# Kernel tuning notes

Hardware: AMD Instinct MI355X
Metric: run time of the kernel (lower is better)

Reference implementation:

```python
import jax, jax.numpy as jnp
import numpy as np

ALPHA = 1.0
ARAP_WEIGHT = 1.0
B, N, K, LATENT, HIDDEN = 16, 20000, 16, 256, 1024


def setup_inputs() -> dict:
    key = jax.random.key(0)
    ks = jax.random.split(key, 8)
    code = jax.random.normal(ks[0], (B, LATENT), jnp.float32)
    W1 = jax.random.normal(ks[1], (LATENT, HIDDEN), jnp.float32) / np.sqrt(LATENT)
    b1 = jnp.zeros((HIDDEN,), jnp.float32)
    W2 = jax.random.normal(ks[2], (HIDDEN, N * 3), jnp.float32) / np.sqrt(HIDDEN)
    b2 = jnp.zeros((N * 3,), jnp.float32)
    xyz1 = jax.random.normal(ks[3], (B, N, 3), jnp.float32)
    weightMatrix = jax.random.uniform(ks[4], (N, K), jnp.float32)
    area = jax.random.uniform(ks[5], (N,), jnp.float32)
    neighborsMatrix = jax.random.randint(ks[6], (N, K), 0, N, jnp.int32)
    numNeighbors = jax.random.randint(ks[7], (N,), 1, K + 1, jnp.int32)
    return {"code": code, "W1": W1, "b1": b1, "W2": W2, "b2": b2,
            "xyz1": xyz1, "weightMatrix": weightMatrix, "area": area,
            "neighborsMatrix": neighborsMatrix, "numNeighbors": numNeighbors}


def _mean_energy(code, W1, b1, W2, b2, xyz1, weightMatrix, area,
                 neighborsMatrix, numNeighbors):
    # decoder: MLP latent -> hidden -> N*3, reshaped to [B,N,3]
    h = jax.nn.relu(code @ W1 + b1)
    recon = (h @ W2 + b2).reshape(B, N, 3)

    # mask out padded neighbor slots, fold into weights  [N,K]
    mask = (jnp.arange(K)[None, :] < numNeighbors[:, None]).astype(jnp.float32)
    wm = weightMatrix * mask

    # neighbor-gathered edge vectors: rest pose d, deformed dq  [B,N,K,3]
    d = xyz1[:, :, None, :] - xyz1[:, neighborsMatrix, :]
    dq = recon[:, :, None, :] - recon[:, neighborsMatrix, :]

    # per-vertex weighted covariance and best-fit rotation (Procrustes)
    S = jnp.einsum('nk,bnki,bnkj->bnij', wm, d, dq)          # [B,N,3,3]
    U, s, Vt = jnp.linalg.svd(S)
    V = jnp.swapaxes(Vt, -1, -2)
    Ut = jnp.swapaxes(U, -1, -2)
    det = jnp.linalg.det(V @ Ut)                              # [B,N]
    Vf = V.at[..., :, -1].multiply(jnp.sign(det)[..., None])  # reflection fix
    R = jax.lax.stop_gradient(Vf @ Ut)                        # R treated as constant

    resid = dq - jnp.einsum('bnij,bnkj->bnki', R, d)          # [B,N,K,3]
    e = (ARAP_WEIGHT * ALPHA) * area[None, :, None] * wm[None] \
        * jnp.sum(resid * resid, axis=-1)                     # [B,N,K]
    # torch.mean(torch.mean(e, 2), 1)
    return jnp.mean(e, axis=(1, 2))                           # [B]


def reference(code, W1, b1, W2, b2, xyz1, weightMatrix, area,
              neighborsMatrix, numNeighbors):
    meanEnergy = _mean_energy(code, W1, b1, W2, b2, xyz1, weightMatrix, area,
                              neighborsMatrix, numNeighbors)
    # meanEnergy.backward(ones) -> grad of sum(meanEnergy) wrt code
    code_grad = jax.grad(lambda c: jnp.sum(
        _mean_energy(c, W1, b1, W2, b2, xyz1, weightMatrix, area,
                     neighborsMatrix, numNeighbors)))(code)
    return (meanEnergy, code_grad)
```

## Files before the change

### kernel.cpp

```cpp
#include <hip/hip_runtime.h>

constexpr int B_ = 16;
constexpr int NV = 20000;
constexpr int KN = 16;
constexpr int LAT = 256;
constexpr int HID = 1024;
constexpr int N3 = 60000;
constexpr int RCAP = 64;
constexpr int NCHUNK = 8;
constexpr float INV_NK = 1.0f / (20000.0f * 16.0f);

constexpr size_t H_OFF      = 0;
constexpr size_t XYZT_OFF   = H_OFF + B_ * HID;
constexpr size_t RECONT_OFF = XYZT_OFF + (size_t)N3 * 16;
constexpr size_t GRECON_OFF = RECONT_OFF + (size_t)N3 * 16;
constexpr size_t GH_OFF     = GRECON_OFF + (size_t)B_ * N3;
constexpr size_t RBUF_OFF   = GH_OFF + B_ * HID;
constexpr size_t RCOUNT_OFF = RBUF_OFF + (size_t)NV * 12 * 16;
constexpr size_t RLIST_OFF  = RCOUNT_OFF + NV;
constexpr size_t PART_OFF   = RLIST_OFF + (size_t)NV * RCAP;

__device__ __forceinline__ void atomAddF(float* p, float v) {
  unsafeAtomicAdd(p, v);
}

__global__ __launch_bounds__(256) void k_mlp1(
    const float* __restrict__ code, const float* __restrict__ W1,
    const float* __restrict__ b1, float* __restrict__ h) {
  int t = blockIdx.x * 256 + threadIdx.x;
  int b = t >> 10, hd = t & 1023;
  const float* c = code + b * LAT;
  float acc = b1[hd];
  #pragma unroll 4
  for (int l = 0; l < LAT; ++l) acc += c[l] * W1[l * HID + hd];
  h[t] = fmaxf(acc, 0.0f);
}

__global__ __launch_bounds__(256) void k_xpose(
    const float* __restrict__ xyz, float* __restrict__ xyzT) {
  __shared__ float sm[64][17];
  const int tid = threadIdx.x;
  const int n30 = blockIdx.x * 64;
  {
    const int n3l = tid & 63, bq = tid >> 6;
    #pragma unroll
    for (int p = 0; p < 4; ++p) {
      int b = p * 4 + bq;
      if (n30 + n3l < N3) sm[n3l][b] = xyz[(size_t)b * N3 + n30 + n3l];
    }
  }
  __syncthreads();
  {
    const int b = tid & 15, nq = tid >> 4;
    #pragma unroll
    for (int p = 0; p < 4; ++p) {
      int n3l = p * 16 + nq;
      if (n30 + n3l < N3) xyzT[(size_t)(n30 + n3l) * 16 + b] = sm[n3l][b];
    }
  }
}

__global__ __launch_bounds__(256) void k_mlp2(
    const float* __restrict__ h, const float* __restrict__ W2,
    float* __restrict__ part) {
  __shared__ float hs[16][128];
  const int tid = threadIdx.x;
  const int hd0 = blockIdx.y * 128;
  #pragma unroll
  for (int r = 0; r < 8; ++r) {
    int idx = r * 256 + tid;
    int bb = idx >> 7, cc = idx & 127;
    hs[bb][cc] = h[bb * HID + hd0 + cc];
  }
  __syncthreads();

  const int j4 = blockIdx.x * 1024 + tid * 4;
  if (j4 >= N3) return;

  float4 acc[16];
  #pragma unroll
  for (int b = 0; b < 16; ++b) acc[b] = make_float4(0.f, 0.f, 0.f, 0.f);

  const float* wp = W2 + (size_t)hd0 * N3 + j4;
  float4 w0 = *(const float4*)(wp);
  float4 w1 = *(const float4*)(wp + (size_t)N3);
  float4 w2 = *(const float4*)(wp + (size_t)2 * N3);
  float4 w3 = *(const float4*)(wp + (size_t)3 * N3);

  for (int g = 0; g < 32; ++g) {
    const float* np = wp + (size_t)4 * N3;
    float4 n0, n1, n2, n3;
    if (g < 31) {
      n0 = *(const float4*)(np);
      n1 = *(const float4*)(np + (size_t)N3);
      n2 = *(const float4*)(np + (size_t)2 * N3);
      n3 = *(const float4*)(np + (size_t)3 * N3);
    }
    #pragma unroll
    for (int b = 0; b < 16; ++b) {
      float4 hb = *(const float4*)&hs[b][g * 4];
      acc[b].x += hb.x * w0.x + hb.y * w1.x + hb.z * w2.x + hb.w * w3.x;
      acc[b].y += hb.x * w0.y + hb.y * w1.y + hb.z * w2.y + hb.w * w3.y;
      acc[b].z += hb.x * w0.z + hb.y * w1.z + hb.z * w2.z + hb.w * w3.z;
      acc[b].w += hb.x * w0.w + hb.y * w1.w + hb.z * w2.w + hb.w * w3.w;
    }
    wp = np; w0 = n0; w1 = n1; w2 = n2; w3 = n3;
  }

  float ac[4][16];
  #pragma unroll
  for (int b = 0; b < 16; ++b) {
    ac[0][b] = acc[b].x; ac[1][b] = acc[b].y;
    ac[2][b] = acc[b].z; ac[3][b] = acc[b].w;
  }
  float* pbase = part + ((size_t)blockIdx.y * N3 + j4) * 16;
  #pragma unroll
  for (int jj = 0; jj < 4; ++jj)
    #pragma unroll
    for (int q = 0; q < 4; ++q)
      *(float4*)(pbase + jj * 16 + q * 4) = make_float4(
          ac[jj][q*4+0], ac[jj][q*4+1], ac[jj][q*4+2], ac[jj][q*4+3]);
}

__global__ __launch_bounds__(256) void k_reduce(
    const float* __restrict__ part, const float* __restrict__ b2,
    float* __restrict__ reconT) {
  int t = blockIdx.x * 256 + threadIdx.x;
  if (t >= N3 * 16 / 4) return;
  size_t pos = (size_t)t * 4;
  int j = t >> 2;
  float4 s = *(const float4*)(part + pos);
  #pragma unroll
  for (int c = 1; c < NCHUNK; ++c) {
    float4 p = *(const float4*)(part + (size_t)c * N3 * 16 + pos);
    s.x += p.x; s.y += p.y; s.z += p.z; s.w += p.w;
  }
  float bias = b2[j];
  s.x += bias; s.y += bias; s.z += bias; s.w += bias;
  *(float4*)(reconT + pos) = s;
}

__global__ __launch_bounds__(256) void k_fill(
    const int* __restrict__ nbrs, const int* __restrict__ nnbr,
    int* __restrict__ rcount, int* __restrict__ rlist) {
  int e = blockIdx.x * 256 + threadIdx.x;
  int n = e >> 4, k = e & 15;
  if (k < nnbr[n]) {
    int v = nbrs[e];
    int slot = atomicAdd(&rcount[v], 1);
    if (slot < RCAP) rlist[v * RCAP + slot] = e;
  }
}

__global__ __launch_bounds__(256, 2) void k_rot(
    const float* __restrict__ xT, const float* __restrict__ qT,
    const float* __restrict__ wmat, const float* __restrict__ area,
    const int* __restrict__ nbrs, const int* __restrict__ nnbr,
    float* __restrict__ Rbuf, float* __restrict__ energy) {
  __shared__ float red[64];
  const int tid = threadIdx.x;
  const int b = tid & 15, nl = tid >> 4;
  const int n = blockIdx.x * 16 + nl;
  const int nn = nnbr[n];
  const float ar = area[n];
  const float x0 = xT[(size_t)n*48 + b],      x1 = xT[(size_t)n*48 + 16 + b],
              x2 = xT[(size_t)n*48 + 32 + b];
  const float q0 = qT[(size_t)n*48 + b],      q1 = qT[(size_t)n*48 + 16 + b],
              q2 = qT[(size_t)n*48 + 32 + b];

  float dX[KN], dY[KN], dZ[KN], eX[KN], eY[KN], eZ[KN], wk[KN];
  float S00=0,S01=0,S02=0,S10=0,S11=0,S12=0,S20=0,S21=0,S22=0;
  #pragma unroll
  for (int k = 0; k < KN; ++k) {
    float w=0, dx=0, dy=0, dz=0, ex=0, ey=0, ez=0;
    if (k < nn) {
      int m = nbrs[n * KN + k];
      w = wmat[n * KN + k];
      size_t mb = (size_t)m * 48 + b;
      dx = x0 - xT[mb]; dy = x1 - xT[mb + 16]; dz = x2 - xT[mb + 32];
      ex = q0 - qT[mb]; ey = q1 - qT[mb + 16]; ez = q2 - qT[mb + 32];
    }
    wk[k]=w; dX[k]=dx; dY[k]=dy; dZ[k]=dz; eX[k]=ex; eY[k]=ey; eZ[k]=ez;
    S00 += w*dx*ex; S01 += w*dx*ey; S02 += w*dx*ez;
    S10 += w*dy*ex; S11 += w*dy*ey; S12 += w*dy*ez;
    S20 += w*dz*ex; S21 += w*dz*ey; S22 += w*dz*ez;
  }

  float A00 = S00*S00 + S10*S10 + S20*S20;
  float A01 = S00*S01 + S10*S11 + S20*S21;
  float A02 = S00*S02 + S10*S12 + S20*S22;
  float A11 = S01*S01 + S11*S11 + S21*S21;
  float A12 = S01*S02 + S11*S12 + S21*S22;
  float A22 = S02*S02 + S12*S12 + S22*S22;
  float V00=1,V01=0,V02=0, V10=0,V11=1,V12=0, V20=0,V21=0,V22=1;

  auto rot = [&](float& app, float& aqq, float& apq, float& arp, float& arq,
                 float& vp0, float& vp1, float& vp2,
                 float& vq0, float& vq1, float& vq2) {
    float a = apq;
    if (fabsf(a) > 1e-37f) {
      float tau = (aqq - app) * 0.5f / a;
      float t = copysignf(1.0f, tau) / (fabsf(tau) + sqrtf(1.0f + tau * tau));
      float c = rsqrtf(1.0f + t * t);
      float s = t * c;
      float napp = c*c*app - 2.0f*s*c*a + s*s*aqq;
      float naqq = s*s*app + 2.0f*s*c*a + c*c*aqq;
      app = napp; aqq = naqq; apq = 0.0f;
      float rp = arp, rq = arq;
      arp = c*rp - s*rq; arq = s*rp + c*rq;
      float t0, t1;
      t0=vp0; t1=vq0; vp0 = c*t0 - s*t1; vq0 = s*t0 + c*t1;
      t0=vp1; t1=vq1; vp1 = c*t0 - s*t1; vq1 = s*t0 + c*t1;
      t0=vp2; t1=vq2; vp2 = c*t0 - s*t1; vq2 = s*t0 + c*t1;
    }
  };
  #pragma unroll
  for (int sweep = 0; sweep < 6; ++sweep) {
    rot(A00,A11,A01, A02,A12, V00,V10,V20, V01,V11,V21);
    rot(A00,A22,A02, A01,A12, V00,V10,V20, V02,V12,V22);
    rot(A11,A22,A12, A01,A02, V01,V11,V21, V02,V12,V22);
  }
  auto sw = [](float& a, float& c) { float t = a; a = c; c = t; };
  if (A00 < A11) { sw(A00,A11); sw(V00,V01); sw(V10,V11); sw(V20,V21); }
  if (A00 < A22) { sw(A00,A22); sw(V00,V02); sw(V10,V12); sw(V20,V22); }
  if (A11 < A22) { sw(A11,A22); sw(V01,V02); sw(V11,V12); sw(V21,V22); }

  float v1x=V00, v1y=V10, v1z=V20;
  float v2x=V01, v2y=V11, v2z=V21;

  float u1x = S00*v1x + S01*v1y + S02*v1z;
  float u1y = S10*v1x + S11*v1y + S12*v1z;
  float u1z = S20*v1x + S21*v1y + S22*v1z;
  float s1sq = u1x*u1x + u1y*u1y + u1z*u1z;
  if (s1sq > 1e-30f) { float r = rsqrtf(s1sq); u1x*=r; u1y*=r; u1z*=r; }
  else { u1x = 1.0f; u1y = 0.0f; u1z = 0.0f; }

  float u2x = S00*v2x + S01*v2y + S02*v2z;
  float u2y = S10*v2x + S11*v2y + S12*v2z;
  float u2z = S20*v2x + S21*v2y + S22*v2z;
  float pr = u2x*u1x + u2y*u1y + u2z*u1z;
  u2x -= pr*u1x; u2y -= pr*u1y; u2z -= pr*u1z;
  float s2sq = u2x*u2x + u2y*u2y + u2z*u2z;
  if (s2sq > 1e-12f * s1sq + 1e-30f) {
    float r = rsqrtf(s2sq); u2x*=r; u2y*=r; u2z*=r;
  } else {
    float ex_ = (fabsf(u1x) < 0.9f) ? 1.0f : 0.0f;
    float ey_ = 1.0f - ex_;
    float pp = ex_*u1x + ey_*u1y;
    u2x = ex_ - pp*u1x; u2y = ey_ - pp*u1y; u2z = -pp*u1z;
    float r = rsqrtf(u2x*u2x + u2y*u2y + u2z*u2z);
    u2x*=r; u2y*=r; u2z*=r;
  }
  float u3x = u1y*u2z - u1z*u2y, u3y = u1z*u2x - u1x*u2z, u3z = u1x*u2y - u1y*u2x;
  float v3x = v1y*v2z - v1z*v2y, v3y = v1z*v2x - v1x*v2z, v3z = v1x*v2y - v1y*v2x;

  float R00 = v1x*u1x + v2x*u2x + v3x*u3x;
  float R01 = v1x*u1y + v2x*u2y + v3x*u3y;
  float R02 = v1x*u1z + v2x*u2z + v3x*u3z;
  float R10 = v1y*u1x + v2y*u2x + v3y*u3x;
  float R11 = v1y*u1y + v2y*u2y + v3y*u3y;
  float R12 = v1y*u1z + v2y*u2z + v3y*u3z;
  float R20 = v1z*u1x + v2z*u2x + v3z*u3x;
  float R21 = v1z*u1y + v2z*u2y + v3z*u3y;
  float R22 = v1z*u1z + v2z*u2z + v3z*u3z;

  float esum = 0, go0 = 0, go1 = 0, go2 = 0;
  const float gf = 2.0f * ar * INV_NK;
  #pragma unroll
  for (int k = 0; k < KN; ++k) {
    float w = wk[k];
    float dx = dX[k], dy = dY[k], dz = dZ[k];
    float rx = eX[k] - (R00*dx + R01*dy + R02*dz);
    float ry = eY[k] - (R10*dx + R11*dy + R12*dz);
    float rz = eZ[k] - (R20*dx + R21*dy + R22*dz);
    esum += w * (rx*rx + ry*ry + rz*rz);
    float gc = gf * w;
    go0 += gc*rx; go1 += gc*ry; go2 += gc*rz;
  }
  esum *= ar * INV_NK;

  float* rb = Rbuf + (size_t)n * 192 + b;
  rb[0]=R00;  rb[16]=R01;  rb[32]=R02;
  rb[48]=R10; rb[64]=R11;  rb[80]=R12;
  rb[96]=R20; rb[112]=R21; rb[128]=R22;
  rb[144]=go0; rb[160]=go1; rb[176]=go2;

  esum += __shfl_down(esum, 32);
  esum += __shfl_down(esum, 16);
  int wave = tid >> 6, lane = tid & 63;
  if (lane < 16) red[wave * 16 + lane] = esum;
  __syncthreads();
  if (tid < 16) atomAddF(&energy[tid], red[tid] + red[16 + tid] + red[32 + tid] + red[48 + tid]);
}

__global__ __launch_bounds__(256) void k_scatter(
    const float* __restrict__ xT, const float* __restrict__ qT,
    const float* __restrict__ wmat, const float* __restrict__ area,
    const float* __restrict__ Rbuf, const int* __restrict__ rcount,
    const int* __restrict__ rlist, float* __restrict__ grecon) {
  int t = blockIdx.x * 256 + threadIdx.x;
  int v = t >> 4, b = t & 15;
  const float xv0 = xT[(size_t)v*48 + b], xv1 = xT[(size_t)v*48 + 16 + b],
              xv2 = xT[(size_t)v*48 + 32 + b];
  const float qv0 = qT[(size_t)v*48 + b], qv1 = qT[(size_t)v*48 + 16 + b],
              qv2 = qT[(size_t)v*48 + 32 + b];
  float g0 = 0, g1 = 0, g2 = 0;
  int deg = min(rcount[v], RCAP);
  for (int i = 0; i < deg; ++i) {
    int e = rlist[v * RCAP + i];
    int n = e >> 4;
    float gc = 2.0f * INV_NK * area[n] * wmat[e];
    const float* rb = Rbuf + (size_t)n * 192 + b;
    size_t nb = (size_t)n * 48 + b;
    float dx = xT[nb] - xv0, dy = xT[nb+16] - xv1, dz = xT[nb+32] - xv2;
    float ex = qT[nb] - qv0, ey = qT[nb+16] - qv1, ez = qT[nb+32] - qv2;
    float rx = ex - (rb[0]*dx  + rb[16]*dy  + rb[32]*dz);
    float ry = ey - (rb[48]*dx + rb[64]*dy  + rb[80]*dz);
    float rz = ez - (rb[96]*dx + rb[112]*dy + rb[128]*dz);
    g0 -= gc*rx; g1 -= gc*ry; g2 -= gc*rz;
  }
  const float* ob = Rbuf + (size_t)v * 192 + b;
  g0 += ob[144]; g1 += ob[160]; g2 += ob[176];
  float* gq = grecon + (size_t)b * N3 + v * 3;
  gq[0] = g0; gq[1] = g1; gq[2] = g2;
}

__global__ __launch_bounds__(256, 2) void k_mlp2_bwd(
    const float* __restrict__ gr, const float* __restrict__ W2,
    float* __restrict__ gh) {
  const int tid = threadIdx.x;
  const int lane = tid & 63;
  const int wv = tid >> 6;
  const int laneJ = lane & 15, laneR = lane >> 4;
  const int row0 = blockIdx.y * 32 + wv * 8 + laneR * 2;

  float4 acc0[16], acc1[16];
  #pragma unroll
  for (int b = 0; b < 16; ++b) {
    acc0[b] = make_float4(0.f, 0.f, 0.f, 0.f);
    acc1[b] = make_float4(0.f, 0.f, 0.f, 0.f);
  }

  const int jbase = blockIdx.x * 64 + laneJ * 4;
  const float* w2r0 = W2 + (size_t)row0 * N3;
  const float* w2r1 = W2 + (size_t)(row0 + 1) * N3;

  for (int it = 0; it < 59; ++it) {
    int j = jbase + it * 1024;
    if (j < N3) {
      float4 w0 = *(const float4*)(w2r0 + j);
      float4 w1 = *(const float4*)(w2r1 + j);
      #pragma unroll
      for (int b = 0; b < 16; ++b) {
        float4 g = *(const float4*)(gr + (size_t)b * N3 + j);
        acc0[b].x += g.x * w0.x; acc0[b].y += g.y * w0.y;
        acc0[b].z += g.z * w0.z; acc0[b].w += g.w * w0.w;
        acc1[b].x += g.x * w1.x; acc1[b].y += g.y * w1.y;
        acc1[b].z += g.z * w1.z; acc1[b].w += g.w * w1.w;
      }
    }
  }

  float s0[16], s1[16];
  #pragma unroll
  for (int b = 0; b < 16; ++b) {
    s0[b] = (acc0[b].x + acc0[b].y) + (acc0[b].z + acc0[b].w);
    s1[b] = (acc1[b].x + acc1[b].y) + (acc1[b].z + acc1[b].w);
  }
  #pragma unroll
  for (int m = 1; m <= 8; m <<= 1) {
    #pragma unroll
    for (int b = 0; b < 16; ++b) {
      s0[b] += __shfl_xor(s0[b], m);
      s1[b] += __shfl_xor(s1[b], m);
    }
  }
  if (laneJ == 0) {
    #pragma unroll
    for (int b = 0; b < 16; ++b) {
      atomAddF(&gh[b * HID + row0], s0[b]);
      atomAddF(&gh[b * HID + row0 + 1], s1[b]);
    }
  }
}

__global__ __launch_bounds__(256) void k_mlp1_bwd(
    const float* __restrict__ gh, const float* __restrict__ h,
    const float* __restrict__ W1, float* __restrict__ gcode) {
  __shared__ float gm[128];
  const int b = blockIdx.x;
  const int hd0 = blockIdx.y * 128;
  const int l = threadIdx.x;
  if (l < 128) {
    float g = gh[b * HID + hd0 + l];
    gm[l] = (h[b * HID + hd0 + l] > 0.0f) ? g : 0.0f;
  }
  __syncthreads();
  const float4* wp = (const float4*)(W1 + (size_t)l * HID + hd0);
  float acc = 0.0f;
  #pragma unroll
  for (int i = 0; i < 32; ++i) {
    float4 w4 = wp[i];
    acc += w4.x * gm[i*4+0] + w4.y * gm[i*4+1] + w4.z * gm[i*4+2] + w4.w * gm[i*4+3];
  }
  atomAddF(&gcode[b * LAT + l], acc);
}

extern "C" void kernel_launch(void* const* d_in, const int* in_sizes, int n_in,
                              void* d_out, int out_size, void* d_ws, size_t ws_size,
                              hipStream_t stream) {
  const float* code = (const float*)d_in[0];
  const float* W1   = (const float*)d_in[1];
  const float* b1   = (const float*)d_in[2];
  const float* W2   = (const float*)d_in[3];
  const float* b2   = (const float*)d_in[4];
  const float* xyz  = (const float*)d_in[5];
  const float* wmat = (const float*)d_in[6];
  const float* area = (const float*)d_in[7];
  const int* nbrs   = (const int*)d_in[8];
  const int* nnbr   = (const int*)d_in[9];

  float* out = (float*)d_out;
  float* ws = (float*)d_ws;
  float* h      = ws + H_OFF;
  float* xyzT   = ws + XYZT_OFF;
  float* reconT = ws + RECONT_OFF;
  float* grecon = ws + GRECON_OFF;
  float* gh     = ws + GH_OFF;
  float* Rbuf   = ws + RBUF_OFF;
  int*   rcount = (int*)(ws + RCOUNT_OFF);
  int*   rlist  = (int*)(ws + RLIST_OFF);
  float* part   = ws + PART_OFF;

  hipMemsetAsync(gh, 0, (size_t)B_ * HID * sizeof(float), stream);
  hipMemsetAsync(rcount, 0, (size_t)NV * sizeof(int), stream);
  hipMemsetAsync(out, 0, (size_t)(B_ + B_ * LAT) * sizeof(float), stream);

  k_fill<<<dim3(NV * KN / 256), dim3(256), 0, stream>>>(nbrs, nnbr, rcount, rlist);
  k_xpose<<<dim3((N3 + 63) / 64), dim3(256), 0, stream>>>(xyz, xyzT);
  k_mlp1<<<dim3(64), dim3(256), 0, stream>>>(code, W1, b1, h);
  k_mlp2<<<dim3(59, NCHUNK), dim3(256), 0, stream>>>(h, W2, part);
  k_reduce<<<dim3((N3 * 16 / 4 + 255) / 256), dim3(256), 0, stream>>>(part, b2, reconT);
  k_rot<<<dim3(NV / 16), dim3(256), 0, stream>>>(
      xyzT, reconT, wmat, area, nbrs, nnbr, Rbuf, out);
  k_scatter<<<dim3(NV * 16 / 256), dim3(256), 0, stream>>>(
      xyzT, reconT, wmat, area, Rbuf, rcount, rlist, grecon);
  k_mlp2_bwd<<<dim3(16, 32), dim3(256), 0, stream>>>(grecon, W2, gh);
  k_mlp1_bwd<<<dim3(B_, 8), dim3(256), 0, stream>>>(gh, h, W1, out + B_);
}
```

Before: 597.5 us.

## Store per-edge gradient vectors in k_rot and re-split both MLP2 GEMMs

k_rot now writes each edge's weighted residual gradient to a [N*K*48] buffer plus a per-vertex own-gradient, so k_scatter only gathers and sums precomputed vectors instead of recomputing residuals from positions and rotations. Separately, the forward MLP2 split goes from 8 to 16 hidden chunks, and the backward MLP2 kernel handles one row per thread across twice as many blocks. The aim is to cut gather work and raise parallelism, at the cost of writing about 61MB of edge gradients and of more partial sums and atomics.

```diff
diff --git a/kernel.cpp b/kernel.cpp
--- a/kernel.cpp
+++ b/kernel.cpp
@@ -7,7 +7,7 @@
 constexpr int HID = 1024;
 constexpr int N3 = 60000;
 constexpr int RCAP = 64;
-constexpr int NCHUNK = 8;
+constexpr int NCHUNK = 16;
 constexpr float INV_NK = 1.0f / (20000.0f * 16.0f);
 
 constexpr size_t H_OFF      = 0;
@@ -15,8 +15,9 @@
 constexpr size_t RECONT_OFF = XYZT_OFF + (size_t)N3 * 16;
 constexpr size_t GRECON_OFF = RECONT_OFF + (size_t)N3 * 16;
 constexpr size_t GH_OFF     = GRECON_OFF + (size_t)B_ * N3;
-constexpr size_t RBUF_OFF   = GH_OFF + B_ * HID;
-constexpr size_t RCOUNT_OFF = RBUF_OFF + (size_t)NV * 12 * 16;
+constexpr size_t GVEC_OFF   = GH_OFF + B_ * HID;
+constexpr size_t OWN_OFF    = GVEC_OFF + (size_t)NV * KN * 48;
+constexpr size_t RCOUNT_OFF = OWN_OFF + (size_t)NV * 48;
 constexpr size_t RLIST_OFF  = RCOUNT_OFF + NV;
 constexpr size_t PART_OFF   = RLIST_OFF + (size_t)NV * RCAP;
 
@@ -63,13 +64,13 @@
 __global__ __launch_bounds__(256) void k_mlp2(
     const float* __restrict__ h, const float* __restrict__ W2,
     float* __restrict__ part) {
-  __shared__ float hs[16][128];
+  __shared__ float hs[16][64];
   const int tid = threadIdx.x;
-  const int hd0 = blockIdx.y * 128;
-  #pragma unroll
-  for (int r = 0; r < 8; ++r) {
+  const int hd0 = blockIdx.y * 64;
+  #pragma unroll
+  for (int r = 0; r < 4; ++r) {
     int idx = r * 256 + tid;
-    int bb = idx >> 7, cc = idx & 127;
+    int bb = idx >> 6, cc = idx & 63;
     hs[bb][cc] = h[bb * HID + hd0 + cc];
   }
   __syncthreads();
@@ -87,10 +88,10 @@
   float4 w2 = *(const float4*)(wp + (size_t)2 * N3);
   float4 w3 = *(const float4*)(wp + (size_t)3 * N3);
 
-  for (int g = 0; g < 32; ++g) {
+  for (int g = 0; g < 16; ++g) {
     const float* np = wp + (size_t)4 * N3;
     float4 n0, n1, n2, n3;
-    if (g < 31) {
+    if (g < 15) {
       n0 = *(const float4*)(np);
       n1 = *(const float4*)(np + (size_t)N3);
       n2 = *(const float4*)(np + (size_t)2 * N3);
@@ -156,7 +157,8 @@
     const float* __restrict__ xT, const float* __restrict__ qT,
     const float* __restrict__ wmat, const float* __restrict__ area,
     const int* __restrict__ nbrs, const int* __restrict__ nnbr,
-    float* __restrict__ Rbuf, float* __restrict__ energy) {
+    float* __restrict__ gvec, float* __restrict__ own,
+    float* __restrict__ energy) {
   __shared__ float red[64];
   const int tid = threadIdx.x;
   const int b = tid & 15, nl = tid >> 4;
@@ -275,15 +277,15 @@
     float rz = eZ[k] - (R20*dx + R21*dy + R22*dz);
     esum += w * (rx*rx + ry*ry + rz*rz);
     float gc = gf * w;
-    go0 += gc*rx; go1 += gc*ry; go2 += gc*rz;
+    float cx = gc*rx, cy = gc*ry, cz = gc*rz;
+    go0 += cx; go1 += cy; go2 += cz;
+    float* gp = gvec + (size_t)(n * KN + k) * 48 + b;
+    gp[0] = cx; gp[16] = cy; gp[32] = cz;
   }
   esum *= ar * INV_NK;
 
-  float* rb = Rbuf + (size_t)n * 192 + b;
-  rb[0]=R00;  rb[16]=R01;  rb[32]=R02;
-  rb[48]=R10; rb[64]=R11;  rb[80]=R12;
-  rb[96]=R20; rb[112]=R21; rb[128]=R22;
-  rb[144]=go0; rb[160]=go1; rb[176]=go2;
+  float* ob = own + (size_t)n * 48 + b;
+  ob[0] = go0; ob[16] = go1; ob[32] = go2;
 
   esum += __shfl_down(esum, 32);
   esum += __shfl_down(esum, 16);
@@ -294,93 +296,59 @@
 }
 
 __global__ __launch_bounds__(256) void k_scatter(
-    const float* __restrict__ xT, const float* __restrict__ qT,
-    const float* __restrict__ wmat, const float* __restrict__ area,
-    const float* __restrict__ Rbuf, const int* __restrict__ rcount,
-    const int* __restrict__ rlist, float* __restrict__ grecon) {
+    const float* __restrict__ gvec, const float* __restrict__ own,
+    const int* __restrict__ rcount, const int* __restrict__ rlist,
+    float* __restrict__ grecon) {
   int t = blockIdx.x * 256 + threadIdx.x;
   int v = t >> 4, b = t & 15;
-  const float xv0 = xT[(size_t)v*48 + b], xv1 = xT[(size_t)v*48 + 16 + b],
-              xv2 = xT[(size_t)v*48 + 32 + b];
-  const float qv0 = qT[(size_t)v*48 + b], qv1 = qT[(size_t)v*48 + 16 + b],
-              qv2 = qT[(size_t)v*48 + 32 + b];
-  float g0 = 0, g1 = 0, g2 = 0;
+  const float* ob = own + (size_t)v * 48 + b;
+  float g0 = ob[0], g1 = ob[16], g2 = ob[32];
   int deg = min(rcount[v], RCAP);
   for (int i = 0; i < deg; ++i) {
     int e = rlist[v * RCAP + i];
-    int n = e >> 4;
-    float gc = 2.0f * INV_NK * area[n] * wmat[e];
-    const float* rb = Rbuf + (size_t)n * 192 + b;
-    size_t nb = (size_t)n * 48 + b;
-    float dx = xT[nb] - xv0, dy = xT[nb+16] - xv1, dz = xT[nb+32] - xv2;
-    float ex = qT[nb] - qv0, ey = qT[nb+16] - qv1, ez = qT[nb+32] - qv2;
-    float rx = ex - (rb[0]*dx  + rb[16]*dy  + rb[32]*dz);
-    float ry = ey - (rb[48]*dx + rb[64]*dy  + rb[80]*dz);
-    float rz = ez - (rb[96]*dx + rb[112]*dy + rb[128]*dz);
-    g0 -= gc*rx; g1 -= gc*ry; g2 -= gc*rz;
-  }
-  const float* ob = Rbuf + (size_t)v * 192 + b;
-  g0 += ob[144]; g1 += ob[160]; g2 += ob[176];
+    const float* gp = gvec + (size_t)e * 48 + b;
+    g0 -= gp[0]; g1 -= gp[16]; g2 -= gp[32];
+  }
   float* gq = grecon + (size_t)b * N3 + v * 3;
   gq[0] = g0; gq[1] = g1; gq[2] = g2;
 }
 
-__global__ __launch_bounds__(256, 2) void k_mlp2_bwd(
+__global__ __launch_bounds__(256) void k_mlp2_bwd(
     const float* __restrict__ gr, const float* __restrict__ W2,
     float* __restrict__ gh) {
   const int tid = threadIdx.x;
   const int lane = tid & 63;
   const int wv = tid >> 6;
   const int laneJ = lane & 15, laneR = lane >> 4;
-  const int row0 = blockIdx.y * 32 + wv * 8 + laneR * 2;
-
-  float4 acc0[16], acc1[16];
-  #pragma unroll
-  for (int b = 0; b < 16; ++b) {
-    acc0[b] = make_float4(0.f, 0.f, 0.f, 0.f);
-    acc1[b] = make_float4(0.f, 0.f, 0.f, 0.f);
-  }
+  const int row = blockIdx.y * 16 + wv * 4 + laneR;
+
+  float acc[16];
+  #pragma unroll
+  for (int b = 0; b < 16; ++b) acc[b] = 0.0f;
 
   const int jbase = blockIdx.x * 64 + laneJ * 4;
-  const float* w2r0 = W2 + (size_t)row0 * N3;
-  const float* w2r1 = W2 + (size_t)(row0 + 1) * N3;
+  const float* w2r = W2 + (size_t)row * N3;
 
   for (int it = 0; it < 59; ++it) {
     int j = jbase + it * 1024;
     if (j < N3) {
-      float4 w0 = *(const float4*)(w2r0 + j);
-      float4 w1 = *(const float4*)(w2r1 + j);
+      float4 w = *(const float4*)(w2r + j);
       #pragma unroll
       for (int b = 0; b < 16; ++b) {
         float4 g = *(const float4*)(gr + (size_t)b * N3 + j);
-        acc0[b].x += g.x * w0.x; acc0[b].y += g.y * w0.y;
-        acc0[b].z += g.z * w0.z; acc0[b].w += g.w * w0.w;
-        acc1[b].x += g.x * w1.x; acc1[b].y += g.y * w1.y;
-        acc1[b].z += g.z * w1.z; acc1[b].w += g.w * w1.w;
+        acc[b] += g.x * w.x + g.y * w.y + g.z * w.z + g.w * w.w;
       }
     }
   }
 
-  float s0[16], s1[16];
-  #pragma unroll
-  for (int b = 0; b < 16; ++b) {
-    s0[b] = (acc0[b].x + acc0[b].y) + (acc0[b].z + acc0[b].w);
-    s1[b] = (acc1[b].x + acc1[b].y) + (acc1[b].z + acc1[b].w);
-  }
   #pragma unroll
   for (int m = 1; m <= 8; m <<= 1) {
     #pragma unroll
-    for (int b = 0; b < 16; ++b) {
-      s0[b] += __shfl_xor(s0[b], m);
-      s1[b] += __shfl_xor(s1[b], m);
-    }
+    for (int b = 0; b < 16; ++b) acc[b] += __shfl_xor(acc[b], m);
   }
   if (laneJ == 0) {
     #pragma unroll
-    for (int b = 0; b < 16; ++b) {
-      atomAddF(&gh[b * HID + row0], s0[b]);
-      atomAddF(&gh[b * HID + row0 + 1], s1[b]);
-    }
+    for (int b = 0; b < 16; ++b) atomAddF(&gh[b * HID + row], acc[b]);
   }
 }
 
@@ -427,7 +395,8 @@
   float* reconT = ws + RECONT_OFF;
   float* grecon = ws + GRECON_OFF;
   float* gh     = ws + GH_OFF;
-  float* Rbuf   = ws + RBUF_OFF;
+  float* gvec   = ws + GVEC_OFF;
+  float* own    = ws + OWN_OFF;
   int*   rcount = (int*)(ws + RCOUNT_OFF);
   int*   rlist  = (int*)(ws + RLIST_OFF);
   float* part   = ws + PART_OFF;
@@ -442,9 +411,9 @@
   k_mlp2<<<dim3(59, NCHUNK), dim3(256), 0, stream>>>(h, W2, part);
   k_reduce<<<dim3((N3 * 16 / 4 + 255) / 256), dim3(256), 0, stream>>>(part, b2, reconT);
   k_rot<<<dim3(NV / 16), dim3(256), 0, stream>>>(
-      xyzT, reconT, wmat, area, nbrs, nnbr, Rbuf, out);
+      xyzT, reconT, wmat, area, nbrs, nnbr, gvec, own, out);
   k_scatter<<<dim3(NV * 16 / 256), dim3(256), 0, stream>>>(
-      xyzT, reconT, wmat, area, Rbuf, rcount, rlist, grecon);
-  k_mlp2_bwd<<<dim3(16, 32), dim3(256), 0, stream>>>(grecon, W2, gh);
+      gvec, own, rcount, rlist, grecon);
+  k_mlp2_bwd<<<dim3(16, 64), dim3(256), 0, stream>>>(grecon, W2, gh);
   k_mlp1_bwd<<<dim3(B_, 8), dim3(256), 0, stream>>>(gh, h, W1, out + B_);
 }
```

After: 679.8 us. 13.8% more time.
